# Optimization experiments

Hardware: AMD Instinct MI355X
Metric: run time of the kernel (lower is better)

## Reference

```python
import jax, jax.numpy as jnp
import numpy as np
from functools import lru_cache


@lru_cache(maxsize=None)
def _mw_basis(L):
    """Fully-normalized associated Legendre basis on MW-style theta grid.

    Returns (Pfull, w):
      Pfull: (L, 2L-1, L) float32, Pfull[l, L-1+m, t] = Nbar_lm * P_l^m(cos theta_t)
             (zero for |m| > l), with Y_lm = Pfull * exp(i m phi).
      w:     (L,) float32 quadrature weights sin(theta)*dtheta*dphi.
    """
    t = np.arange(L)
    theta = np.pi * (2 * t + 1) / (2 * L - 1)  # MW theta samples
    ct, st = np.cos(theta), np.sin(theta)
    P = np.zeros((L, L, L))
    P[0, 0] = np.full(L, np.sqrt(1.0 / (4.0 * np.pi)))
    for m in range(1, L):
        P[m, m] = -np.sqrt((2.0 * m + 1.0) / (2.0 * m)) * st * P[m - 1, m - 1]
    for m in range(L - 1):
        P[m + 1, m] = np.sqrt(2.0 * m + 3.0) * ct * P[m, m]
    for m in range(L):
        for l in range(m + 2, L):
            a = np.sqrt((4.0 * l * l - 1.0) / (l * l - m * m))
            b = np.sqrt(((2.0 * l + 1.0) * (l - 1 - m) * (l - 1 + m)) / ((2.0 * l - 3.0) * (l * l - m * m)))
            P[l, m] = a * ct * P[l - 1, m] - b * P[l - 2, m]
    Pfull = np.zeros((L, 2 * L - 1, L), dtype=np.float32)
    for m in range(L):
        Pfull[:, L - 1 + m, :] = P[:, m, :]
        if m > 0:
            Pfull[:, L - 1 - m, :] = ((-1.0) ** m) * P[:, m, :]
    dang = 2.0 * np.pi / (2 * L - 1)  # theta and phi spacing
    w = (st * dang * dang).astype(np.float32)
    return jnp.asarray(Pfull), jnp.asarray(w)


def sht_forward(x):
    """x: (L, 2L-1, C) real -> flm: (L, 2L-1, C) complex, m indexed -(L-1)..(L-1)."""
    L = x.shape[0]
    P, w = _mw_basis(L)
    F = jnp.fft.fft(x.astype(jnp.complex64), axis=1)           # k = 0..2L-2
    F = jnp.concatenate([F[:, L:, :], F[:, :L, :]], axis=1)     # reorder to m = -(L-1)..L-1
    # flm = sum_t w_t Nbar P_l^m(theta_t) * Fm(theta_t)
    return jnp.einsum('lmt,tmc->lmc', P * w[None, None, :], F)


def sht_inverse(flm):
    """flm: (L, 2L-1, C) complex -> f: (L, 2L-1, C) complex on MW grid."""
    L = flm.shape[0]
    P, _ = _mw_basis(L)
    G = jnp.einsum('lmc,lmt->tmc', flm, P)                      # (theta, m, C)
    G = jnp.concatenate([G[:, L - 1:, :], G[:, :L - 1, :]], axis=1)  # m order -> fft k order
    return jnp.fft.ifft(G, axis=1) * (2 * L - 1)


def zero_pad_flm(flm, L_out):
    L_in = flm.shape[0]
    p = L_out - L_in
    return jnp.pad(flm, ((0, p), (p, p), (0, 0)))


L_IN = 256
L_FREQ = 128
L_OUT = 256
C_IN = 32
C_OUT = 32
T_DIM = 256


def setup_inputs() -> dict:
    key = jax.random.key(0)
    ks = jax.random.split(key, 8)
    return {
        'x': jax.random.normal(ks[0], (L_IN, 2 * L_IN - 1, C_IN), jnp.float32),
        't_emb': jax.random.normal(ks[1], (T_DIM,), jnp.float32),
        'weight_real': 0.02 * jax.random.normal(ks[2], (L_FREQ, C_IN, C_OUT), jnp.float32),
        'weight_imag': 0.02 * jax.random.normal(ks[3], (L_FREQ, C_IN, C_OUT), jnp.float32),
        'w_tr': jax.random.normal(ks[4], (T_DIM, L_FREQ), jnp.float32) / np.sqrt(T_DIM),
        'b_tr': jnp.zeros((L_FREQ,), jnp.float32),
        'w_ti': jax.random.normal(ks[5], (T_DIM, L_FREQ), jnp.float32) / np.sqrt(T_DIM),
        'b_ti': jnp.zeros((L_FREQ,), jnp.float32),
    }


def reference(x, t_emb, weight_real, weight_imag, w_tr, b_tr, w_ti, b_ti):
    # forward SHT over all channels at once
    flm = sht_forward(x)                                       # (L_in, 2L_in-1, C_in) complex64
    # bilinear resize of the spectrum to the used bandlimit (real/imag separately)
    tgt = (L_FREQ, 2 * L_FREQ - 1, flm.shape[2])
    flm = (jax.image.resize(jnp.real(flm), tgt, 'bilinear')
           + 1j * jax.image.resize(jnp.imag(flm), tgt, 'bilinear'))
    # time-modulated per-degree complex spectral weights
    t_cplx = (t_emb @ w_tr + b_tr) + 1j * (t_emb @ w_ti + b_ti)   # (L_freq,)
    weight = t_cplx[:, None, None] * (weight_real + 1j * weight_imag)  # (L_freq, C_in, C_out)
    flm = jnp.einsum('lmi,lio->lmo', flm, weight)
    # zero pad to output bandlimit and inverse SHT
    flm = zero_pad_flm(flm, L_OUT)                             # (L_out, 2L_out-1, C_out)
    x_out = jnp.real(sht_inverse(flm))
    return x_out
```

## Files before the change

### kernel.cpp

```cpp
#include <hip/hip_runtime.h>
#include <math.h>

#define PI_D 3.14159265358979323846

typedef short v8s __attribute__((ext_vector_type(8)));
typedef float v4f __attribute__((ext_vector_type(4)));

constexpr size_t OFF_PA   = 0;
constexpr size_t OFF_PT   = 8388608;
constexpr size_t OFF_SFRE = 12582912;
constexpr size_t OFF_SFIM = 14680064;
constexpr size_t OFF_FRE  = 16777216;
constexpr size_t OFF_FIM  = 18874368;
constexpr size_t OFF_CRE  = 20971520;
constexpr size_t OFF_CIM  = 22016000;
constexpr size_t OFF_AF   = 23060480;
constexpr size_t OFF_AI   = 23191552;
constexpr size_t OFF_WQ   = 23322624;
constexpr size_t OFF_TC   = 23322880;
constexpr size_t OFF_WLW  = 23323136;
constexpr size_t OFF_WLI  = 23323648;
constexpr size_t OFF_WMW  = 23324160;
constexpr size_t OFF_WMI  = 23325696;
constexpr size_t OFF_GRE  = OFF_FRE;
constexpr size_t OFF_GIM  = OFF_FIM;

__device__ __forceinline__ short f2bf(float f) {
  unsigned u = __float_as_uint(f);
  unsigned r = (u + 0x7FFFu + ((u >> 16) & 1u)) >> 16;
  return (short)r;
}


__device__ void phase_prep(const float* t_emb, const float* w_tr, const float* b_tr,
                           const float* w_ti, const float* b_ti, float* ws, int g0, int tid) {
  if (g0 < 2048) {
    int g = g0 * 256 + tid;
    bool inv = (g >= 262144);
    int gid = inv ? g - 262144 : g;
    int j = gid & 7, lane = (gid >> 3) & 63, ks = (gid >> 9) & 15, mt = gid >> 13;
    int m = mt * 16 + (lane & 15);
    int k = ks * 32 + ((lane >> 4) << 3) + j;
    float v = 0.f;
    if (!inv) {
      if (k < 511) {
        int mm = (m < 256) ? m : m - 256;
        int kk = (mm * k) % 511;
        float ang = (float)(2.0 * PI_D / 511.0) * (float)kk;
        float s, c; __sincosf(ang, &s, &c);
        v = (m < 256) ? c : -s;
      }
      ((short*)(ws + OFF_AF))[gid] = f2bf(v);
    } else {
      if (m < 511 && k < 510) {
        int jj = (k < 255) ? k : k - 255;
        int jm = jj - 127;
        int kk = ((jm * m) % 511 + 511) % 511;
        float ang = (float)(2.0 * PI_D / 511.0) * (float)kk;
        float s, c; __sincosf(ang, &s, &c);
        v = (k < 255) ? c : -s;
      }
      ((short*)(ws + OFF_AI))[gid] = f2bf(v);
    }
    return;
  }
  if (tid < 256) {
    double theta = PI_D * (2.0 * tid + 1.0) / 511.0;
    double dang = 2.0 * PI_D / 511.0;
    ws[OFF_WQ + tid] = (float)(sin(theta) * dang * dang);
  }
  {
    int h = tid >> 7, o = tid & 127;
    const float* W = h ? w_ti : w_tr;
    float s = h ? b_ti[o] : b_tr[o];
    for (int T = 0; T < 256; ++T) s += t_emb[T] * W[T * 128 + o];
    ws[OFF_TC + h * 128 + o] = s;
  }
  if (tid < 128) {
    double sf = 2.0 * tid + 0.5;
    double wv[4]; int iv[4]; double wsum = 0.0;
    for (int a = 0; a < 4; ++a) {
      int t = 2 * tid - 1 + a;
      double r = 1.0 - fabs(sf - (double)t) * 0.5;
      bool valid = (t >= 0 && t < 256 && r > 0.0);
      wv[a] = valid ? r : 0.0; iv[a] = valid ? t : 0;
      wsum += wv[a];
    }
    for (int a = 0; a < 4; ++a) {
      ws[OFF_WLW + tid * 4 + a] = (float)(wv[a] / wsum);
      ((int*)(ws + OFF_WLI))[tid * 4 + a] = iv[a];
    }
  }
  if (tid < 255) {
    double inv2 = 511.0 / 255.0;
    double sf = (tid + 0.5) * inv2 - 0.5;
    int t0 = (int)floor(sf) - 2;
    double wv[6]; int iv[6]; double wsum = 0.0;
    for (int b = 0; b < 6; ++b) {
      int t = t0 + b;
      double r = 1.0 - fabs(sf - (double)t) * (255.0 / 511.0);
      bool valid = (t >= 0 && t < 511 && r > 0.0);
      wv[b] = valid ? r : 0.0; iv[b] = valid ? t : 0;
      wsum += wv[b];
    }
    for (int b = 0; b < 6; ++b) {
      ws[OFF_WMW + tid * 6 + b] = (float)(wv[b] / wsum);
      ((int*)(ws + OFF_WMI))[tid * 6 + b] = iv[b];
    }
  }
}

__device__ void phase_legendre(float* ws, char* smem, int m, int t) {
  double* cA = (double*)smem;
  double* cB = cA + 256;
  double* cS = cB + 256;
  short* tile = (short*)(smem + 6144);
  short* tileT = (short*)(smem + 6144 + 8960);
  {
    int l = t;
    if (l >= 1) cS[l] = -sqrt((2.0 * l + 1.0) / (2.0 * l));
    if (l >= m + 2) {
      double ll = l, mm = m;
      double den = ll * ll - mm * mm;
      cA[l] = sqrt((4.0 * ll * ll - 1.0) / den);
      cB[l] = sqrt((2.0 * ll + 1.0) * (ll - 1.0 - mm) * (ll - 1.0 + mm) /
                   ((2.0 * ll - 3.0) * den));
    }
  }
  __syncthreads();
  bool wantPT = (m < 128);
  short* PAp = (short*)(ws + OFF_PA) + (size_t)m * 65536;
  short* PTp = (short*)(ws + OFF_PT) + (size_t)m * 65536;
  double theta = PI_D * (2.0 * t + 1.0) / 511.0;
  double ct = cos(theta), st = sin(theta);
  double p0 = sqrt(1.0 / (4.0 * PI_D));
  for (int k = 1; k <= m; ++k) p0 *= cS[k] * st;
  double pm1 = 0.0, pcur = 0.0;
  for (int lt = 0; lt < 16; ++lt) {
    for (int li = 0; li < 16; ++li) {
      int l = lt * 16 + li;
      float v;
      if (l < m) v = 0.f;
      else if (l == m) { pcur = p0; v = (float)pcur; }
      else if (l == m + 1) { pm1 = pcur; pcur = sqrt(2.0 * m + 3.0) * ct * pm1; v = (float)pcur; }
      else { double p2 = cA[l] * ct * pcur - cB[l] * pm1; pm1 = pcur; pcur = p2; v = (float)p2; }
      short bv = f2bf(v);
      tile[li * 280 + t] = bv;
      if (wantPT) tileT[t * 34 + li] = bv;
    }
    __syncthreads();
#pragma unroll
    for (int pass = 0; pass < 2; ++pass) {
      int ch = pass * 256 + t;
      int li = ch & 15, T0 = ch >> 4;
      size_t dst = (size_t)lt * 4096 + (size_t)(T0 >> 2) * 512 + (size_t)((T0 & 3) * 16 + li) * 8;
      *(v8s*)(PAp + dst) = *(const v8s*)(tile + li * 280 + T0 * 8);
    }
    if (wantPT) {
#pragma unroll
      for (int pass = 0; pass < 2; ++pass) {
        int ch = pass * 256 + t;
        int tt = ch >> 1, li0 = (ch & 1) * 8;
        size_t dst = (size_t)(tt >> 4) * 4096 + (size_t)(lt >> 1) * 512 +
                     (size_t)(((lt & 1) * 2 + (li0 >> 3)) * 16 + (tt & 15)) * 8;
        const int* src = (const int*)(tileT + tt * 34 + li0);
        int* d = (int*)(PTp + dst);
        d[0] = src[0]; d[1] = src[1]; d[2] = src[2]; d[3] = src[3];
      }
    }
    __syncthreads();
  }
}

__device__ void phase_gemm_f(const float* x, float* ws, int uid, int tid) {
  int nt = uid & 1, mh = (uid >> 1) & 1, t = uid >> 2;
  int wave = tid >> 6, lane = tid & 63;
  const v8s* A = (const v8s*)(ws + OFF_AF);
  float wq = ws[OFF_WQ + t];
  const float* xb = x + (size_t)t * 511 * 32 + nt * 16 + (lane & 15);
  int phiB = (lane >> 4) << 3;
  int mtB = mh * 16 + wave * 4;
  v4f acc[4];
#pragma unroll
  for (int i = 0; i < 4; ++i) acc[i] = (v4f){0.f, 0.f, 0.f, 0.f};
  float bv[8];
  v8s a_cur[4], a_nxt[4];
#pragma unroll
  for (int j = 0; j < 8; ++j) {
    int phi = phiB + j;
    bv[j] = (phi < 511) ? xb[(size_t)phi * 32] : 0.f;
  }
#pragma unroll
  for (int i = 0; i < 4; ++i) a_cur[i] = A[(size_t)((mtB + i) * 16 + 0) * 64 + lane];
  for (int ks = 0; ks < 16; ++ks) {
    float bn[8];
    if (ks < 15) {
      int phi0 = (ks + 1) * 32 + phiB;
#pragma unroll
      for (int j = 0; j < 8; ++j) {
        int phi = phi0 + j;
        bn[j] = (phi < 511) ? xb[(size_t)phi * 32] : 0.f;
      }
#pragma unroll
      for (int i = 0; i < 4; ++i)
        a_nxt[i] = A[(size_t)((mtB + i) * 16 + ks + 1) * 64 + lane];
    }
    v8s b;
#pragma unroll
    for (int j = 0; j < 8; ++j) b[j] = f2bf(wq * bv[j]);
#pragma unroll
    for (int i = 0; i < 4; ++i)
      acc[i] = __builtin_amdgcn_mfma_f32_16x16x32_bf16(a_cur[i], b, acc[i], 0, 0, 0);
    if (ks < 15) {
#pragma unroll
      for (int j = 0; j < 8; ++j) bv[j] = bn[j];
#pragma unroll
      for (int i = 0; i < 4; ++i) a_cur[i] = a_nxt[i];
    }
  }
  int quad = lane >> 4, cn = nt * 16 + (lane & 15);
#pragma unroll
  for (int i = 0; i < 4; ++i) {
    int mt = mtB + i;
#pragma unroll
    for (int r = 0; r < 4; ++r) {
      int mp = mt * 16 + quad * 4 + r;
      float v = acc[i][r];
      if (mp < 256) ws[OFF_FRE + ((size_t)mp * 256 + t) * 32 + cn] = v;
      else          ws[OFF_FIM + ((size_t)(mp - 256) * 256 + t) * 32 + cn] = v;
    }
  }
}

__device__ void phase_legfwd(float* ws, int uid, int tid) {
  int m = uid >> 2;
  int mt = (uid & 3) * 4 + (tid >> 6), lane = tid & 63;
  const v8s* A = (const v8s*)(ws + OFF_PA) + (size_t)m * 8192;
  int cl = lane & 15, tB = (lane >> 4) << 3;
  int quad = lane >> 4;
  v4f acc[4];
#pragma unroll
  for (int n = 0; n < 4; ++n) acc[n] = (v4f){0.f, 0.f, 0.f, 0.f};
  bool sk = (mt * 16 + 15) < m;
  if (!sk) {
    const float* Fb[4];
#pragma unroll
    for (int n = 0; n < 4; ++n) {
      int cp = n * 16 + cl;
      Fb[n] = ws + (cp < 32 ? OFF_FRE : OFF_FIM) + (size_t)m * 8192 + (size_t)tB * 32 + (cp & 31);
    }
    float bv[4][8];
    v8s a_cur = A[(size_t)mt * 512 + lane];
#pragma unroll
    for (int n = 0; n < 4; ++n)
#pragma unroll
      for (int j = 0; j < 8; ++j) bv[n][j] = Fb[n][(size_t)j * 32];
    for (int ks = 0; ks < 8; ++ks) {
      float bn[4][8];
      v8s a_nxt;
      if (ks < 7) {
#pragma unroll
        for (int n = 0; n < 4; ++n)
#pragma unroll
          for (int j = 0; j < 8; ++j) bn[n][j] = Fb[n][(size_t)((ks + 1) * 32 + j) * 32];
        a_nxt = A[(size_t)mt * 512 + (ks + 1) * 64 + lane];
      }
#pragma unroll
      for (int n = 0; n < 4; ++n) {
        v8s b;
#pragma unroll
        for (int j = 0; j < 8; ++j) b[j] = f2bf(bv[n][j]);
        acc[n] = __builtin_amdgcn_mfma_f32_16x16x32_bf16(a_cur, b, acc[n], 0, 0, 0);
      }
      if (ks < 7) {
#pragma unroll
        for (int n = 0; n < 4; ++n)
#pragma unroll
          for (int j = 0; j < 8; ++j) bv[n][j] = bn[n][j];
        a_cur = a_nxt;
      }
    }
  }
#pragma unroll
  for (int n = 0; n < 4; ++n) {
    int cp = n * 16 + cl;
    float* dst = ws + ((cp >= 32) ? OFF_SFIM : OFF_SFRE) + (size_t)m * 8192 + (cp & 31);
#pragma unroll
    for (int r = 0; r < 4; ++r) {
      int l = mt * 16 + quad * 4 + r;
      dst[(size_t)l * 32] = sk ? 0.f : acc[n][r];
    }
  }
}

__device__ void phase_conv(const float* w_real, const float* w_imag, float* ws, char* smem,
                           int uid, int tid) {
  int l = uid >> 3, jq8 = uid & 7;
  int jl = tid >> 5, o = tid & 31;
  float* wr = (float*)smem;
  float* wi = wr + 32 * 36;
  float* fr = wi + 32 * 36;
  float* fi = fr + 8 * 32;
  {
    int oo = tid >> 3, i4 = (tid & 7) * 4;
    float tcr = ws[OFF_TC + l], tci = ws[OFF_TC + 128 + l];
#pragma unroll
    for (int q = 0; q < 4; ++q) {
      int i = i4 + q;
      float a = w_real[(size_t)l * 1024 + i * 32 + oo];
      float b = w_imag[(size_t)l * 1024 + i * 32 + oo];
      wr[oo * 36 + i] = tcr * a - tci * b;
      wi[oo * 36 + i] = tcr * b + tci * a;
    }
  }
  const float* SFRE = ws + OFF_SFRE;
  const float* SFIM = ws + OFF_SFIM;
  const float* WMW = ws + OFF_WMW;
  const int* WMI = (const int*)(ws + OFF_WMI);
  float wl[4]; int liv[4];
#pragma unroll
  for (int a = 0; a < 4; ++a) {
    wl[a] = ws[OFF_WLW + l * 4 + a];
    liv[a] = ((const int*)(ws + OFF_WLI))[l * 4 + a];
  }
  for (int ji = 0; ji < 4; ++ji) {
    int j = jq8 * 32 + ji * 8 + jl;
    int jp = (j < 255) ? j : 254;
    float accr = 0.f, acci = 0.f;
    for (int b = 0; b < 6; ++b) {
      float wm = WMW[jp * 6 + b];
      int jm = WMI[jp * 6 + b];
      bool mneg = (jm < 255);
      int mm = mneg ? (255 - jm) : (jm - 255);
      float fre_f = (mneg && (mm & 1)) ? -1.f : 1.f;
      float fim_f = mneg ? -fre_f : 1.f;
#pragma unroll
      for (int a = 0; a < 4; ++a) {
        float w = wm * wl[a];
        size_t base = ((size_t)mm * 256 + liv[a]) * 32 + o;
        accr = fmaf(w * fre_f, SFRE[base], accr);
        acci = fmaf(w * fim_f, SFIM[base], acci);
      }
    }
    __syncthreads();
    fr[jl * 32 + o] = accr;
    fi[jl * 32 + o] = acci;
    __syncthreads();
    float sr = 0.f, si = 0.f;
#pragma unroll
    for (int i0 = 0; i0 < 32; i0 += 4) {
      float4 f_r = *(const float4*)(fr + jl * 32 + i0);
      float4 f_i = *(const float4*)(fi + jl * 32 + i0);
      float4 w_r = *(const float4*)(wr + o * 36 + i0);
      float4 w_i = *(const float4*)(wi + o * 36 + i0);
      sr += f_r.x * w_r.x - f_i.x * w_i.x;  si += f_r.x * w_i.x + f_i.x * w_r.x;
      sr += f_r.y * w_r.y - f_i.y * w_i.y;  si += f_r.y * w_i.y + f_i.y * w_r.y;
      sr += f_r.z * w_r.z - f_i.z * w_i.z;  si += f_r.z * w_i.z + f_i.z * w_r.z;
      sr += f_r.w * w_r.w - f_i.w * w_i.w;  si += f_r.w * w_i.w + f_i.w * w_r.w;
    }
    if (j < 255) {
      float s = (j < 127 && ((127 - j) & 1)) ? -1.f : 1.f;
      ws[OFF_CRE + ((size_t)j * 128 + l) * 32 + o] = s * sr;
      ws[OFF_CIM + ((size_t)j * 128 + l) * 32 + o] = s * si;
    }
  }
}

__device__ void phase_linv(float* ws, int uid, int tid) {
  int j = uid >> 2;
  int d = j - 127; int mm = (d < 0) ? -d : d;
  int mt = (uid & 3) * 4 + (tid >> 6), lane = tid & 63;
  const v8s* A = (const v8s*)(ws + OFF_PT) + (size_t)mm * 8192;
  int cl = lane & 15, lB = (lane >> 4) << 3;
  int quad = lane >> 4;
  v4f acc[4];
#pragma unroll
  for (int n = 0; n < 4; ++n) acc[n] = (v4f){0.f, 0.f, 0.f, 0.f};
  int ks0 = mm >> 5;
  const float* Cb[4];
#pragma unroll
  for (int n = 0; n < 4; ++n) {
    int cp = n * 16 + cl;
    Cb[n] = ws + (cp < 32 ? OFF_CRE : OFF_CIM) + ((size_t)j * 128 + lB) * 32 + (cp & 31);
  }
  float bv[4][8];
  v8s a_cur = A[(size_t)mt * 512 + ks0 * 64 + lane];
#pragma unroll
  for (int n = 0; n < 4; ++n)
#pragma unroll
    for (int j8 = 0; j8 < 8; ++j8) bv[n][j8] = Cb[n][(size_t)(ks0 * 32 + j8) * 32];
  for (int ks = ks0; ks < 4; ++ks) {
    float bn[4][8];
    v8s a_nxt;
    if (ks < 3) {
#pragma unroll
      for (int n = 0; n < 4; ++n)
#pragma unroll
        for (int j8 = 0; j8 < 8; ++j8) bn[n][j8] = Cb[n][(size_t)((ks + 1) * 32 + j8) * 32];
      a_nxt = A[(size_t)mt * 512 + (ks + 1) * 64 + lane];
    }
#pragma unroll
    for (int n = 0; n < 4; ++n) {
      v8s b;
#pragma unroll
      for (int j8 = 0; j8 < 8; ++j8) b[j8] = f2bf(bv[n][j8]);
      acc[n] = __builtin_amdgcn_mfma_f32_16x16x32_bf16(a_cur, b, acc[n], 0, 0, 0);
    }
    if (ks < 3) {
#pragma unroll
      for (int n = 0; n < 4; ++n)
#pragma unroll
        for (int j8 = 0; j8 < 8; ++j8) bv[n][j8] = bn[n][j8];
      a_cur = a_nxt;
    }
  }
#pragma unroll
  for (int n = 0; n < 4; ++n) {
    int cp = n * 16 + cl;
    float* dst = ws + ((cp >= 32) ? OFF_GIM : OFF_GRE) + (size_t)(cp & 31);
#pragma unroll
    for (int r = 0; r < 4; ++r) {
      int t = mt * 16 + quad * 4 + r;
      dst[((size_t)t * 255 + j) * 32] = acc[n][r];
    }
  }
}

__device__ void phase_gemm_i(const float* ws, float* out, int uid, int tid) {
  int nt = uid & 1, mh = (uid >> 1) & 1, t = uid >> 2;
  int wave = tid >> 6, lane = tid & 63;
  const v8s* A = (const v8s*)(ws + OFF_AI);
  const float* GRE = ws + OFF_GRE;
  const float* GIM = ws + OFF_GIM;
  int mtB = mh * 16 + wave * 4;
  int cn = nt * 16 + (lane & 15);
  int kB = (lane >> 4) << 3;
  v4f acc[4];
#pragma unroll
  for (int i = 0; i < 4; ++i) acc[i] = (v4f){0.f, 0.f, 0.f, 0.f};
  float bv[8];
  v8s a_cur[4], a_nxt[4];
#pragma unroll
  for (int j8 = 0; j8 < 8; ++j8) {
    int k = kB + j8;
    float v = 0.f;
    if (k < 255)      v = GRE[((size_t)t * 255 + k) * 32 + cn];
    else if (k < 510) v = GIM[((size_t)t * 255 + (k - 255)) * 32 + cn];
    bv[j8] = v;
  }
#pragma unroll
  for (int i = 0; i < 4; ++i) a_cur[i] = A[(size_t)((mtB + i) * 16 + 0) * 64 + lane];
  for (int ks = 0; ks < 16; ++ks) {
    float bn[8];
    if (ks < 15) {
      int k0 = (ks + 1) * 32 + kB;
#pragma unroll
      for (int j8 = 0; j8 < 8; ++j8) {
        int k = k0 + j8;
        float v = 0.f;
        if (k < 255)      v = GRE[((size_t)t * 255 + k) * 32 + cn];
        else if (k < 510) v = GIM[((size_t)t * 255 + (k - 255)) * 32 + cn];
        bn[j8] = v;
      }
#pragma unroll
      for (int i = 0; i < 4; ++i)
        a_nxt[i] = A[(size_t)((mtB + i) * 16 + ks + 1) * 64 + lane];
    }
    v8s b;
#pragma unroll
    for (int j8 = 0; j8 < 8; ++j8) b[j8] = f2bf(bv[j8]);
#pragma unroll
    for (int i = 0; i < 4; ++i)
      acc[i] = __builtin_amdgcn_mfma_f32_16x16x32_bf16(a_cur[i], b, acc[i], 0, 0, 0);
    if (ks < 15) {
#pragma unroll
      for (int j8 = 0; j8 < 8; ++j8) bv[j8] = bn[j8];
#pragma unroll
      for (int i = 0; i < 4; ++i) a_cur[i] = a_nxt[i];
    }
  }
  int quad = lane >> 4;
#pragma unroll
  for (int i = 0; i < 4; ++i) {
    int mt = mtB + i;
#pragma unroll
    for (int r = 0; r < 4; ++r) {
      int phi = mt * 16 + quad * 4 + r;
      if (phi < 511) out[((size_t)t * 511 + phi) * 32 + cn] = acc[i][r];
    }
  }
}

__global__ __launch_bounds__(256) void k_prepleg(const float* t_emb, const float* w_tr,
                                                 const float* b_tr, const float* w_ti,
                                                 const float* b_ti, float* ws) {
  __shared__ __align__(16) char smem[32768];
  int bid = blockIdx.x;
  if (bid < 2049) phase_prep(t_emb, w_tr, b_tr, w_ti, b_ti, ws, bid, threadIdx.x);
  else phase_legendre(ws, smem, bid - 2049, threadIdx.x);
}
__global__ __launch_bounds__(256) void kw_gemm_f(const float* x, float* ws) {
  phase_gemm_f(x, ws, blockIdx.x, threadIdx.x);
}
__global__ __launch_bounds__(256) void kw_legfwd(float* ws) {
  phase_legfwd(ws, blockIdx.x, threadIdx.x);
}
__global__ __launch_bounds__(256) void kw_conv(const float* w_real, const float* w_imag, float* ws) {
  __shared__ __align__(16) char smem[32768];
  phase_conv(w_real, w_imag, ws, smem, blockIdx.x, threadIdx.x);
}
__global__ __launch_bounds__(256) void kw_linv(float* ws) {
  phase_linv(ws, blockIdx.x, threadIdx.x);
}
__global__ __launch_bounds__(256) void kw_gemm_i(const float* ws, float* out) {
  phase_gemm_i(ws, out, blockIdx.x, threadIdx.x);
}

extern "C" void kernel_launch(void* const* d_in, const int* in_sizes, int n_in,
                              void* d_out, int out_size, void* d_ws, size_t ws_size,
                              hipStream_t stream) {
  const float* x = (const float*)d_in[0];
  const float* t_emb = (const float*)d_in[1];
  const float* w_real = (const float*)d_in[2];
  const float* w_imag = (const float*)d_in[3];
  const float* w_tr = (const float*)d_in[4];
  const float* b_tr = (const float*)d_in[5];
  const float* w_ti = (const float*)d_in[6];
  const float* b_ti = (const float*)d_in[7];
  float* ws = (float*)d_ws;
  float* out = (float*)d_out;
  (void)in_sizes; (void)n_in; (void)out_size; (void)ws_size;

  hipLaunchKernelGGL(k_prepleg, dim3(2305), dim3(256), 0, stream,
                     t_emb, w_tr, b_tr, w_ti, b_ti, ws);
  hipLaunchKernelGGL(kw_gemm_f, dim3(1024), dim3(256), 0, stream, x, ws);
  hipLaunchKernelGGL(kw_legfwd, dim3(1024), dim3(256), 0, stream, ws);
  hipLaunchKernelGGL(kw_conv, dim3(1024), dim3(256), 0, stream, w_real, w_imag, ws);
  hipLaunchKernelGGL(kw_linv, dim3(1020), dim3(256), 0, stream, ws);
  hipLaunchKernelGGL(kw_gemm_i, dim3(1024), dim3(256), 0, stream, ws, out);
}
```

Baseline: 198.1 us.

## Stage B operands through shared memory with double-buffered bf16 tiles

In the forward/inverse phi GEMMs and the forward Legendre GEMM, each block now loads its B operand cooperatively with coalesced loads, converts it to bf16 once, and writes it into a double-buffered LDS tile. MFMA fragments are then read from LDS. Before, every wave did its own strided, redundant global loads and conversions. The Legendre kernel also returns early with zeros for quarter-blocks that lie entirely below m. Smaller changes put the Legendre blocks first in the prep kernel and shrink the conv kernel's shared buffer. The cost is a __syncthreads per k-step and extra LDS traffic.

```diff
diff --git a/kernel.cpp b/kernel.cpp
--- a/kernel.cpp
+++ b/kernel.cpp
@@ -172,53 +172,52 @@
   }
 }
 
-__device__ void phase_gemm_f(const float* x, float* ws, int uid, int tid) {
+__device__ void phase_gemm_f(const float* x, float* ws, short* lds, int uid, int tid) {
   int nt = uid & 1, mh = (uid >> 1) & 1, t = uid >> 2;
   int wave = tid >> 6, lane = tid & 63;
   const v8s* A = (const v8s*)(ws + OFF_AF);
   float wq = ws[OFF_WQ + t];
-  const float* xb = x + (size_t)t * 511 * 32 + nt * 16 + (lane & 15);
-  int phiB = (lane >> 4) << 3;
+  const float* row = x + (size_t)t * 511 * 32 + nt * 16;
+  int cl = lane & 15, quad = lane >> 4;
   int mtB = mh * 16 + wave * 4;
+  int ck = tid >> 4, cc = tid & 15;
   v4f acc[4];
 #pragma unroll
   for (int i = 0; i < 4; ++i) acc[i] = (v4f){0.f, 0.f, 0.f, 0.f};
-  float bv[8];
   v8s a_cur[4], a_nxt[4];
 #pragma unroll
-  for (int j = 0; j < 8; ++j) {
-    int phi = phiB + j;
-    bv[j] = (phi < 511) ? xb[(size_t)phi * 32] : 0.f;
-  }
-#pragma unroll
   for (int i = 0; i < 4; ++i) a_cur[i] = A[(size_t)((mtB + i) * 16 + 0) * 64 + lane];
+  {
+    float p0 = wq * row[(size_t)ck * 32 + cc];
+    float p1 = wq * row[(size_t)(ck + 16) * 32 + cc];
+    lds[cc * 40 + ck] = f2bf(p0);
+    lds[cc * 40 + ck + 16] = f2bf(p1);
+  }
+  __syncthreads();
   for (int ks = 0; ks < 16; ++ks) {
-    float bn[8];
+    float n0 = 0.f, n1 = 0.f;
     if (ks < 15) {
-      int phi0 = (ks + 1) * 32 + phiB;
-#pragma unroll
-      for (int j = 0; j < 8; ++j) {
-        int phi = phi0 + j;
-        bn[j] = (phi < 511) ? xb[(size_t)phi * 32] : 0.f;
-      }
+      int ph0 = (ks + 1) * 32 + ck, ph1 = ph0 + 16;
+      n0 = (ph0 < 511) ? wq * row[(size_t)ph0 * 32 + cc] : 0.f;
+      n1 = (ph1 < 511) ? wq * row[(size_t)ph1 * 32 + cc] : 0.f;
 #pragma unroll
       for (int i = 0; i < 4; ++i)
         a_nxt[i] = A[(size_t)((mtB + i) * 16 + ks + 1) * 64 + lane];
     }
-    v8s b;
-#pragma unroll
-    for (int j = 0; j < 8; ++j) b[j] = f2bf(wq * bv[j]);
+    v8s b = *(const v8s*)(lds + (ks & 1) * 640 + cl * 40 + quad * 8);
 #pragma unroll
     for (int i = 0; i < 4; ++i)
       acc[i] = __builtin_amdgcn_mfma_f32_16x16x32_bf16(a_cur[i], b, acc[i], 0, 0, 0);
     if (ks < 15) {
-#pragma unroll
-      for (int j = 0; j < 8; ++j) bv[j] = bn[j];
+      short* nb = lds + ((ks + 1) & 1) * 640;
+      nb[cc * 40 + ck] = f2bf(n0);
+      nb[cc * 40 + ck + 16] = f2bf(n1);
 #pragma unroll
       for (int i = 0; i < 4; ++i) a_cur[i] = a_nxt[i];
-    }
-  }
-  int quad = lane >> 4, cn = nt * 16 + (lane & 15);
+      __syncthreads();
+    }
+  }
+  int cn = nt * 16 + cl;
 #pragma unroll
   for (int i = 0; i < 4; ++i) {
     int mt = mtB + i;
@@ -232,53 +231,69 @@
   }
 }
 
-__device__ void phase_legfwd(float* ws, int uid, int tid) {
-  int m = uid >> 2;
-  int mt = (uid & 3) * 4 + (tid >> 6), lane = tid & 63;
-  const v8s* A = (const v8s*)(ws + OFF_PA) + (size_t)m * 8192;
-  int cl = lane & 15, tB = (lane >> 4) << 3;
-  int quad = lane >> 4;
-  v4f acc[4];
-#pragma unroll
-  for (int n = 0; n < 4; ++n) acc[n] = (v4f){0.f, 0.f, 0.f, 0.f};
-  bool sk = (mt * 16 + 15) < m;
-  if (!sk) {
-    const float* Fb[4];
+__device__ void phase_legfwd(float* ws, short* lds, int uid, int tid) {
+  int m = uid >> 2, q = uid & 3;
+  int lane = tid & 63;
+  int cl = lane & 15, quad = lane >> 4;
+  if (q * 64 + 63 < m) {
+    int mt = q * 4 + (tid >> 6);
 #pragma unroll
     for (int n = 0; n < 4; ++n) {
       int cp = n * 16 + cl;
-      Fb[n] = ws + (cp < 32 ? OFF_FRE : OFF_FIM) + (size_t)m * 8192 + (size_t)tB * 32 + (cp & 31);
-    }
-    float bv[4][8];
-    v8s a_cur = A[(size_t)mt * 512 + lane];
-#pragma unroll
-    for (int n = 0; n < 4; ++n)
-#pragma unroll
-      for (int j = 0; j < 8; ++j) bv[n][j] = Fb[n][(size_t)j * 32];
-    for (int ks = 0; ks < 8; ++ks) {
-      float bn[4][8];
-      v8s a_nxt;
-      if (ks < 7) {
-#pragma unroll
-        for (int n = 0; n < 4; ++n)
-#pragma unroll
-          for (int j = 0; j < 8; ++j) bn[n][j] = Fb[n][(size_t)((ks + 1) * 32 + j) * 32];
-        a_nxt = A[(size_t)mt * 512 + (ks + 1) * 64 + lane];
+      float* dst = ws + ((cp >= 32) ? OFF_SFIM : OFF_SFRE) + (size_t)m * 8192 + (cp & 31);
+#pragma unroll
+      for (int r = 0; r < 4; ++r) {
+        int l = mt * 16 + quad * 4 + r;
+        dst[(size_t)l * 32] = 0.f;
       }
+    }
+    return;
+  }
+  int mt = q * 4 + (tid >> 6);
+  bool sk = (mt * 16 + 15) < m;
+  const v8s* A = (const v8s*)(ws + OFF_PA) + (size_t)m * 8192;
+  int half = (tid >> 5) & 1, c = tid & 31, tb = tid >> 6;
+  const float* srcb = ws + (half ? OFF_FIM : OFF_FRE) + (size_t)m * 8192 + c;
+  short* myrow = lds;
+  int ldsw = (half * 32 + c) * 40 + tb;
+  v4f acc[4];
+#pragma unroll
+  for (int n = 0; n < 4; ++n) acc[n] = (v4f){0.f, 0.f, 0.f, 0.f};
+  v8s a_cur = A[(size_t)mt * 512 + lane];
+  v8s a_nxt;
+  {
+    float pv[8];
+#pragma unroll
+    for (int pass = 0; pass < 8; ++pass)
+      pv[pass] = srcb[(size_t)(pass * 4 + tb) * 32];
+#pragma unroll
+    for (int pass = 0; pass < 8; ++pass)
+      myrow[ldsw + pass * 4] = f2bf(pv[pass]);
+  }
+  __syncthreads();
+  for (int ks = 0; ks < 8; ++ks) {
+    float pn[8];
+    if (ks < 7) {
+#pragma unroll
+      for (int pass = 0; pass < 8; ++pass)
+        pn[pass] = srcb[(size_t)((ks + 1) * 32 + pass * 4 + tb) * 32];
+      a_nxt = A[(size_t)mt * 512 + (ks + 1) * 64 + lane];
+    }
+    const short* cur = lds + (ks & 1) * 2560;
+    if (!sk) {
 #pragma unroll
       for (int n = 0; n < 4; ++n) {
-        v8s b;
-#pragma unroll
-        for (int j = 0; j < 8; ++j) b[j] = f2bf(bv[n][j]);
+        v8s b = *(const v8s*)(cur + (n * 16 + cl) * 40 + quad * 8);
         acc[n] = __builtin_amdgcn_mfma_f32_16x16x32_bf16(a_cur, b, acc[n], 0, 0, 0);
       }
-      if (ks < 7) {
-#pragma unroll
-        for (int n = 0; n < 4; ++n)
-#pragma unroll
-          for (int j = 0; j < 8; ++j) bv[n][j] = bn[n][j];
-        a_cur = a_nxt;
-      }
+    }
+    if (ks < 7) {
+      short* nb = lds + ((ks + 1) & 1) * 2560;
+#pragma unroll
+      for (int pass = 0; pass < 8; ++pass)
+        nb[ldsw + pass * 4] = f2bf(pn[pass]);
+      a_cur = a_nxt;
+      __syncthreads();
     }
   }
 #pragma unroll
@@ -426,60 +441,55 @@
   }
 }
 
-__device__ void phase_gemm_i(const float* ws, float* out, int uid, int tid) {
+__device__ void phase_gemm_i(const float* ws, float* out, short* lds, int uid, int tid) {
   int nt = uid & 1, mh = (uid >> 1) & 1, t = uid >> 2;
   int wave = tid >> 6, lane = tid & 63;
   const v8s* A = (const v8s*)(ws + OFF_AI);
   const float* GRE = ws + OFF_GRE;
   const float* GIM = ws + OFF_GIM;
+  int cl = lane & 15, quad = lane >> 4;
   int mtB = mh * 16 + wave * 4;
-  int cn = nt * 16 + (lane & 15);
-  int kB = (lane >> 4) << 3;
+  int cn = nt * 16 + cl;
+  int ck = tid >> 4, cc = tid & 15;
+  int ccg = nt * 16 + cc;
   v4f acc[4];
 #pragma unroll
   for (int i = 0; i < 4; ++i) acc[i] = (v4f){0.f, 0.f, 0.f, 0.f};
-  float bv[8];
   v8s a_cur[4], a_nxt[4];
 #pragma unroll
-  for (int j8 = 0; j8 < 8; ++j8) {
-    int k = kB + j8;
-    float v = 0.f;
-    if (k < 255)      v = GRE[((size_t)t * 255 + k) * 32 + cn];
-    else if (k < 510) v = GIM[((size_t)t * 255 + (k - 255)) * 32 + cn];
-    bv[j8] = v;
-  }
-#pragma unroll
   for (int i = 0; i < 4; ++i) a_cur[i] = A[(size_t)((mtB + i) * 16 + 0) * 64 + lane];
+  {
+    float p0 = GRE[((size_t)t * 255 + ck) * 32 + ccg];
+    float p1 = GRE[((size_t)t * 255 + ck + 16) * 32 + ccg];
+    lds[cc * 40 + ck] = f2bf(p0);
+    lds[cc * 40 + ck + 16] = f2bf(p1);
+  }
+  __syncthreads();
   for (int ks = 0; ks < 16; ++ks) {
-    float bn[8];
+    float n0 = 0.f, n1 = 0.f;
     if (ks < 15) {
-      int k0 = (ks + 1) * 32 + kB;
-#pragma unroll
-      for (int j8 = 0; j8 < 8; ++j8) {
-        int k = k0 + j8;
-        float v = 0.f;
-        if (k < 255)      v = GRE[((size_t)t * 255 + k) * 32 + cn];
-        else if (k < 510) v = GIM[((size_t)t * 255 + (k - 255)) * 32 + cn];
-        bn[j8] = v;
-      }
+      int k0 = (ks + 1) * 32 + ck, k1 = k0 + 16;
+      if (k0 < 255)      n0 = GRE[((size_t)t * 255 + k0) * 32 + ccg];
+      else if (k0 < 510) n0 = GIM[((size_t)t * 255 + (k0 - 255)) * 32 + ccg];
+      if (k1 < 255)      n1 = GRE[((size_t)t * 255 + k1) * 32 + ccg];
+      else if (k1 < 510) n1 = GIM[((size_t)t * 255 + (k1 - 255)) * 32 + ccg];
 #pragma unroll
       for (int i = 0; i < 4; ++i)
         a_nxt[i] = A[(size_t)((mtB + i) * 16 + ks + 1) * 64 + lane];
     }
-    v8s b;
-#pragma unroll
-    for (int j8 = 0; j8 < 8; ++j8) b[j8] = f2bf(bv[j8]);
+    v8s b = *(const v8s*)(lds + (ks & 1) * 640 + cl * 40 + quad * 8);
 #pragma unroll
     for (int i = 0; i < 4; ++i)
       acc[i] = __builtin_amdgcn_mfma_f32_16x16x32_bf16(a_cur[i], b, acc[i], 0, 0, 0);
     if (ks < 15) {
-#pragma unroll
-      for (int j8 = 0; j8 < 8; ++j8) bv[j8] = bn[j8];
+      short* nb = lds + ((ks + 1) & 1) * 640;
+      nb[cc * 40 + ck] = f2bf(n0);
+      nb[cc * 40 + ck + 16] = f2bf(n1);
 #pragma unroll
       for (int i = 0; i < 4; ++i) a_cur[i] = a_nxt[i];
-    }
-  }
-  int quad = lane >> 4;
+      __syncthreads();
+    }
+  }
 #pragma unroll
   for (int i = 0; i < 4; ++i) {
     int mt = mtB + i;
@@ -496,24 +506,27 @@
                                                  const float* b_ti, float* ws) {
   __shared__ __align__(16) char smem[32768];
   int bid = blockIdx.x;
-  if (bid < 2049) phase_prep(t_emb, w_tr, b_tr, w_ti, b_ti, ws, bid, threadIdx.x);
-  else phase_legendre(ws, smem, bid - 2049, threadIdx.x);
+  if (bid < 256) phase_legendre(ws, smem, bid, threadIdx.x);
+  else phase_prep(t_emb, w_tr, b_tr, w_ti, b_ti, ws, bid - 256, threadIdx.x);
 }
 __global__ __launch_bounds__(256) void kw_gemm_f(const float* x, float* ws) {
-  phase_gemm_f(x, ws, blockIdx.x, threadIdx.x);
+  __shared__ __align__(16) short lds[2 * 640];
+  phase_gemm_f(x, ws, lds, blockIdx.x, threadIdx.x);
 }
 __global__ __launch_bounds__(256) void kw_legfwd(float* ws) {
-  phase_legfwd(ws, blockIdx.x, threadIdx.x);
+  __shared__ __align__(16) short lds[2 * 2560];
+  phase_legfwd(ws, lds, blockIdx.x, threadIdx.x);
 }
 __global__ __launch_bounds__(256) void kw_conv(const float* w_real, const float* w_imag, float* ws) {
-  __shared__ __align__(16) char smem[32768];
+  __shared__ __align__(16) char smem[11264];
   phase_conv(w_real, w_imag, ws, smem, blockIdx.x, threadIdx.x);
 }
 __global__ __launch_bounds__(256) void kw_linv(float* ws) {
   phase_linv(ws, blockIdx.x, threadIdx.x);
 }
 __global__ __launch_bounds__(256) void kw_gemm_i(const float* ws, float* out) {
-  phase_gemm_i(ws, out, blockIdx.x, threadIdx.x);
+  __shared__ __align__(16) short lds[2 * 640];
+  phase_gemm_i(ws, out, lds, blockIdx.x, threadIdx.x);
 }
 
 extern "C" void kernel_launch(void* const* d_in, const int* in_sizes, int n_in,
```

Measured after the change: 188.3 us. 1.05x faster.
